# Optimization experiments

Measured on AMD Instinct MI355X. Metric: run time of the kernel, lower is better.

## Reference

```python
import jax, jax.numpy as jnp
import numpy as np

D_EMB = 256


def setup_inputs() -> dict:
    key = jax.random.key(0)
    ks = jax.random.split(key, 7)
    B, S, d = 4, 4096, D_EMB
    scale = 1.0 / np.sqrt(d)
    return {
        "x": jax.random.normal(ks[0], (B, S, d), jnp.float32),
        "Wqkv": jax.random.normal(ks[1], (d, 3 * d), jnp.float32) * scale,
        "bqkv": jax.random.normal(ks[2], (3 * d,), jnp.float32) * 0.02,
        "Wproj": jax.random.normal(ks[3], (d, d), jnp.float32) * scale,
        "bproj": jax.random.normal(ks[4], (d,), jnp.float32) * 0.02,
        "Wfc": jax.random.normal(ks[5], (d, 1), jnp.float32) * scale,
        "bfc": jax.random.normal(ks[6], (1,), jnp.float32) * 0.02,
    }


def reference(x, Wqkv, bqkv, Wproj, bproj, Wfc, bfc):
    # qkv projection: [B,S,3d] -> split into q,k,v [B,S,d]
    qkv = x @ Wqkv + bqkv
    q, k, v = jnp.split(qkv, 3, axis=2)
    # full attention scores [B,S,S]; note: original applies NO 1/sqrt(d)
    # scaling (dead branch in source), 'traditional' softmax over last dim
    attn_scores = jnp.einsum("bqd,bkd->bqk", q, k)
    attn_weights = jax.nn.softmax(attn_scores, axis=-1)
    y = jnp.einsum("bqk,bkd->bqd", attn_weights, v)
    y = y @ Wproj + bproj
    out = y @ Wfc + bfc  # [B,S,1]
    return out
```

## Files before the change

kernel.cpp:

```cpp
#include <hip/hip_runtime.h>
#include <hip/hip_bf16.h>

#define BQ 4
#define SQ 4096
#define DQ 256
#define N3 768
#define KBLK 64
#define NITER (SQ / KBLK)
#define KHALF (NITER / 2)
#define LOG2E 1.44269504f
#define THR2 11.5415603f

typedef __attribute__((ext_vector_type(8))) _Float16 f16x8;
typedef __attribute__((ext_vector_type(4))) _Float16 f16x4;
typedef __attribute__((ext_vector_type(4))) float f32x4;
typedef __attribute__((ext_vector_type(4))) unsigned int u32x4;

__device__ __forceinline__ short f2h(float f) {
  _Float16 h = (_Float16)f;
  union { _Float16 h; short s; } v; v.h = h;
  return v.s;
}

__device__ __forceinline__ void gload16(const void* g, void* lds) {
  __builtin_amdgcn_global_load_lds(
      (const __attribute__((address_space(1))) unsigned int*)g,
      (__attribute__((address_space(3))) unsigned int*)lds, 16, 0, 0);
}

__global__ __launch_bounds__(256) void prep_kernel(
    const float* __restrict__ Wqkv, const float* __restrict__ Wproj,
    const float* __restrict__ bproj, const float* __restrict__ Wfc,
    const float* __restrict__ bfc, short* __restrict__ W16T,
    float* __restrict__ Wc) {
  const int t = threadIdx.x;
  if (blockIdx.x == 48) {
    __shared__ float wf[256];
    wf[t] = Wfc[t];
    __syncthreads();
    float acc = 0.f;
    for (int j = 0; j < 256; ++j) acc += Wproj[(size_t)t * 256 + j] * wf[j];
    Wc[t] = acc;
    if (t == 0) {
      float c = bfc[0];
      for (int j = 0; j < 256; ++j) c += bproj[j] * wf[j];
      Wc[256] = c;
    }
    return;
  }
  __shared__ float tile[64][65];
  const int nb = (blockIdx.x % 12) * 64;
  const int kb = (blockIdx.x / 12) * 64;
  const int tr = t >> 6, tc = t & 63;
#pragma unroll
  for (int i = 0; i < 16; ++i)
    tile[tr + i * 4][tc] = Wqkv[(size_t)(kb + tr + i * 4) * N3 + nb + tc];
  __syncthreads();
#pragma unroll
  for (int i = 0; i < 16; ++i)
    W16T[(size_t)(nb + tr + i * 4) * 256 + kb + tc] = f2h(tile[tc][tr + i * 4]);
}

__global__ __launch_bounds__(1024, 4) void qkv_kernel(
    const float* __restrict__ x, const short* __restrict__ W16T,
    const float* __restrict__ bqkv, const float* __restrict__ Wc,
    short* __restrict__ Qb, short* __restrict__ Kb, short* __restrict__ u16) {
  __shared__ short xs[64][264];
  __shared__ short ws[2][64][256];
  __shared__ float u_red[4][4][16];
  const int t = threadIdx.x;
  const int l = t & 63, w = t >> 6;
  const int lr = l & 15, lg = l >> 4;
  const int mq = w >> 2, nq = w & 3;
  const int Mbase = blockIdx.x * 64;

#define STAGE_W(BUF, NT)                                                      \
  {                                                                           \
    _Pragma("unroll") for (int i = 0; i < 2; ++i) {                           \
      const int n = w * 4 + i * 2 + (l >> 5);                                 \
      const int gc = (l & 31) ^ (n & 7);                                      \
      gload16(W16T + (size_t)((NT)*64 + n) * 256 + gc * 8,                    \
              &ws[BUF][w * 4 + i * 2][0]);                                    \
    }                                                                         \
  }

  STAGE_W(0, 0);

  {
    const int m = t >> 4, kc = (t & 15) * 16;
    const float* src = x + (size_t)(Mbase + m) * DQ + kc;
    short tmp[16];
#pragma unroll
    for (int i = 0; i < 16; ++i) tmp[i] = f2h(src[i]);
    *(u32x4*)&xs[m][kc] = *(u32x4*)&tmp[0];
    *(u32x4*)&xs[m][kc + 8] = *(u32x4*)&tmp[8];
  }

  float bias_qk[8], bias_u[4], wc_u[4];
#pragma unroll
  for (int i = 0; i < 8; ++i) bias_qk[i] = bqkv[i * 64 + nq * 16 + lr];
#pragma unroll
  for (int i = 0; i < 4; ++i) {
    bias_u[i] = bqkv[512 + i * 64 + nq * 16 + lr];
    wc_u[i] = Wc[i * 64 + nq * 16 + lr];
  }

  __syncthreads();

  unsigned qksto[8][2];
  float upart[4] = {0.f, 0.f, 0.f, 0.f};

#pragma unroll
  for (int nt = 0; nt < 12; ++nt) {
    const int cur = nt & 1;
    if (nt + 1 < 12) {
      STAGE_W(cur ^ 1, nt + 1);
      asm volatile("s_waitcnt vmcnt(2)" ::: "memory");
    } else {
      asm volatile("s_waitcnt vmcnt(0)" ::: "memory");
    }
    __builtin_amdgcn_s_barrier();
    __builtin_amdgcn_sched_barrier(0);

    f32x4 acc = {};
    const char* wR = (const char*)&ws[cur][nq * 16 + lr][0];
#pragma unroll
    for (int kk = 0; kk < 8; ++kk) {
      f16x8 af = *(f16x8*)&xs[mq * 16 + lr][kk * 32 + lg * 8];
      f16x8 bfr = *(const f16x8*)(wR + (((4 * kk + lg) ^ (lr & 7)) << 4));
      acc = __builtin_amdgcn_mfma_f32_16x16x32_f16(af, bfr, acc, 0, 0, 0);
    }
    if (nt < 8) {
      const float sc = (nt < 4) ? 1.f : LOG2E;
      unsigned s0 = (unsigned short)f2h((acc[0] + bias_qk[nt]) * sc);
      unsigned s1 = (unsigned short)f2h((acc[1] + bias_qk[nt]) * sc);
      unsigned s2 = (unsigned short)f2h((acc[2] + bias_qk[nt]) * sc);
      unsigned s3 = (unsigned short)f2h((acc[3] + bias_qk[nt]) * sc);
      qksto[nt][0] = s0 | (s1 << 16);
      qksto[nt][1] = s2 | (s3 << 16);
    } else {
#pragma unroll
      for (int r = 0; r < 4; ++r) upart[r] += (acc[r] + bias_u[nt - 8]) * wc_u[nt - 8];
    }
    __builtin_amdgcn_s_barrier();
  }

#pragma unroll
  for (int nt = 0; nt < 8; ++nt) {
    const int col = nt * 64 + nq * 16 + lr;
#pragma unroll
    for (int r = 0; r < 4; ++r) {
      const int row = Mbase + mq * 16 + lg * 4 + r;
      const short sv = (short)((qksto[nt][r >> 1] >> ((r & 1) * 16)) & 0xFFFF);
      if (col < 256) Qb[(size_t)row * DQ + col] = sv;
      else           Kb[(size_t)row * DQ + (col - 256)] = sv;
    }
  }

#pragma unroll
  for (int mask = 1; mask <= 8; mask <<= 1)
#pragma unroll
    for (int r = 0; r < 4; ++r) upart[r] += __shfl_xor(upart[r], mask, 64);
  if (lr == 0) {
#pragma unroll
    for (int r = 0; r < 4; ++r) u_red[mq][nq][lg * 4 + r] = upart[r];
  }
  __syncthreads();
  if (t < 64)
    u16[Mbase + t] = f2h(u_red[t >> 4][0][t & 15] + u_red[t >> 4][1][t & 15] +
                         u_red[t >> 4][2][t & 15] + u_red[t >> 4][3][t & 15]);
#undef STAGE_W
}

__global__ __launch_bounds__(256, 2) void attn_kernel(
    const short* __restrict__ Qb, const short* __restrict__ Kb,
    const short* __restrict__ u16, float* __restrict__ Pm,
    float* __restrict__ Pd, float* __restrict__ Pn) {
  __shared__ short Ks[2][64][256];
  __shared__ __align__(16) short u_lds[2048];
  __shared__ float Mrg[4][64][3];

  const int t = threadIdx.x;
  const int l = t & 63, w = t >> 6;
  const int lr = l & 15, lg = l >> 4;
  const int bid = blockIdx.x;
  const int b = bid & 3;
  const int half = (bid >> 2) & 1;
  const int qbase = (bid >> 3) * 64;

  const short* kbase = Kb + ((size_t)b * SQ + (size_t)half * (SQ / 2)) * DQ;
  const short* ubase = u16 + (size_t)b * SQ + half * (SQ / 2);

#define STAGE(BUF, KB)                                                      \
  {                                                                         \
    _Pragma("unroll") for (int i = 0; i < 8; ++i) {                         \
      const int kr = w * 16 + i * 2 + (l >> 5);                             \
      const int gc = (l & 31) ^ (kr & 7);                                   \
      gload16(kbase + (size_t)((KB)*64 + kr) * DQ + gc * 8,                 \
              &Ks[BUF][w * 16 + i * 2][0]);                                 \
    }                                                                       \
  }

  {
    const short* qsrc = Qb + (size_t)(b * SQ + qbase) * DQ;
#pragma unroll
    for (int i = 0; i < 8; ++i) {
      const int qr = w * 16 + i * 2 + (l >> 5);
      const int gc = (l & 31) ^ (qr & 7);
      gload16(qsrc + (size_t)qr * DQ + gc * 8, &Ks[0][w * 16 + i * 2][0]);
    }
  }
  gload16(ubase + w * 512 + (l << 3), &u_lds[w * 512]);

  int koff[8];
#pragma unroll
  for (int kk = 0; kk < 8; ++kk) koff[kk] = ((4 * kk + lg) ^ (lr & 7)) << 4;

  asm volatile("s_waitcnt vmcnt(0)" ::: "memory");
  __syncthreads();

  f16x8 qf[4][8];
#pragma unroll
  for (int mm = 0; mm < 4; ++mm) {
    const char* qR = (const char*)&Ks[0][mm * 16 + lr][0];
#pragma unroll
    for (int kk = 0; kk < 8; ++kk)
      qf[mm][kk] = *(const f16x8*)(qR + koff[kk]);
  }
  __syncthreads();

  float m_run[4] = {-1e30f, -1e30f, -1e30f, -1e30f};
  f32x4 numden[4] = {};

  STAGE(0, 0);

  for (int kb = 0; kb < KHALF; ++kb) {
    const int cur = kb & 1;
    asm volatile("s_waitcnt vmcnt(0)" ::: "memory");
    __builtin_amdgcn_s_barrier();
    __builtin_amdgcn_sched_barrier(0);
    if (kb + 1 < KHALF) STAGE(cur ^ 1, kb + 1);

    const char* kR = (const char*)&Ks[cur][w * 16 + lr][0];
    f32x4 s[4] = {};
    __builtin_amdgcn_s_setprio(1);
#pragma unroll
    for (int kk = 0; kk < 8; ++kk) {
      f16x8 kf = *(const f16x8*)(kR + koff[kk]);
      s[0] = __builtin_amdgcn_mfma_f32_16x16x32_f16(kf, qf[0][kk], s[0], 0, 0, 0);
      s[1] = __builtin_amdgcn_mfma_f32_16x16x32_f16(kf, qf[1][kk], s[1], 0, 0, 0);
      s[2] = __builtin_amdgcn_mfma_f32_16x16x32_f16(kf, qf[2][kk], s[2], 0, 0, 0);
      s[3] = __builtin_amdgcn_mfma_f32_16x16x32_f16(kf, qf[3][kk], s[3], 0, 0, 0);
    }
    __builtin_amdgcn_s_setprio(0);

    float mx[4];
#pragma unroll
    for (int mm = 0; mm < 4; ++mm)
      mx[mm] = fmaxf(fmaxf(s[mm][0], s[mm][1]), fmaxf(s[mm][2], s[mm][3]));
    const bool over = (mx[0] > m_run[0] + THR2) || (mx[1] > m_run[1] + THR2) ||
                      (mx[2] > m_run[2] + THR2) || (mx[3] > m_run[3] + THR2);
    if (__any(over)) {
#pragma unroll
      for (int mm = 0; mm < 4; ++mm) {
        float mt = mx[mm];
        mt = fmaxf(mt, __shfl_xor(mt, 16, 64));
        mt = fmaxf(mt, __shfl_xor(mt, 32, 64));
        const float mn = fmaxf(m_run[mm], mt);
        const float sc = __builtin_amdgcn_exp2f(m_run[mm] - mn);
        m_run[mm] = mn;
#pragma unroll
        for (int r = 0; r < 4; ++r) numden[mm][r] *= sc;
      }
    }

    f16x4 uf;
    {
      const f16x4 uraw = *(const f16x4*)&u_lds[kb * 64 + w * 16 + lg * 4];
#pragma unroll
      for (int j = 0; j < 4; ++j)
        uf[j] = (lr == 0) ? uraw[j]
                          : ((lr == 1) ? (_Float16)1.0f : (_Float16)0.0f);
    }

#pragma unroll
    for (int mm = 0; mm < 4; ++mm) {
      const float p0 = __builtin_amdgcn_exp2f(s[mm][0] - m_run[mm]);
      const float p1 = __builtin_amdgcn_exp2f(s[mm][1] - m_run[mm]);
      const float p2 = __builtin_amdgcn_exp2f(s[mm][2] - m_run[mm]);
      const float p3 = __builtin_amdgcn_exp2f(s[mm][3] - m_run[mm]);
      const auto lo = __builtin_amdgcn_cvt_pkrtz(p0, p1);
      const auto hi = __builtin_amdgcn_cvt_pkrtz(p2, p3);
      f16x4 pf;
      pf[0] = (_Float16)lo[0]; pf[1] = (_Float16)lo[1];
      pf[2] = (_Float16)hi[0]; pf[3] = (_Float16)hi[1];
      numden[mm] = __builtin_amdgcn_mfma_f32_16x16x16f16(uf, pf, numden[mm], 0, 0, 0);
    }
  }

  if (lg == 0) {
#pragma unroll
    for (int mm = 0; mm < 4; ++mm) {
      Mrg[w][mm * 16 + lr][0] = m_run[mm];
      Mrg[w][mm * 16 + lr][1] = numden[mm][1];
      Mrg[w][mm * 16 + lr][2] = numden[mm][0];
    }
  }
  __syncthreads();

  if (t < 64) {
    float M = Mrg[0][t][0];
#pragma unroll
    for (int hh = 1; hh < 4; ++hh) M = fmaxf(M, Mrg[hh][t][0]);
    float dt = 0.f, nt = 0.f;
#pragma unroll
    for (int hh = 0; hh < 4; ++hh) {
      const float e = __builtin_amdgcn_exp2f(Mrg[hh][t][0] - M);
      dt += e * Mrg[hh][t][1];
      nt += e * Mrg[hh][t][2];
    }
    const size_t idx = (size_t)half * (BQ * SQ) + (size_t)b * SQ + qbase + t;
    Pm[idx] = M; Pd[idx] = dt; Pn[idx] = nt;
  }
#undef STAGE
}

__global__ void merge_kernel(const float* __restrict__ Pm,
                             const float* __restrict__ Pd,
                             const float* __restrict__ Pn,
                             const float* __restrict__ Wc,
                             float* __restrict__ out) {
  const int gid = blockIdx.x * 256 + threadIdx.x;
  const float m0 = Pm[gid], m1 = Pm[BQ * SQ + gid];
  const float M = fmaxf(m0, m1);
  const float e0 = __builtin_amdgcn_exp2f(m0 - M);
  const float e1 = __builtin_amdgcn_exp2f(m1 - M);
  const float den = e0 * Pd[gid] + e1 * Pd[BQ * SQ + gid];
  const float num = e0 * Pn[gid] + e1 * Pn[BQ * SQ + gid];
  out[gid] = num / den + Wc[256];
}

extern "C" void kernel_launch(void* const* d_in, const int* in_sizes, int n_in,
                              void* d_out, int out_size, void* d_ws, size_t ws_size,
                              hipStream_t stream) {
  const float* x     = (const float*)d_in[0];
  const float* Wqkv  = (const float*)d_in[1];
  const float* bqkv  = (const float*)d_in[2];
  const float* Wproj = (const float*)d_in[3];
  const float* bproj = (const float*)d_in[4];
  const float* Wfc   = (const float*)d_in[5];
  const float* bfc   = (const float*)d_in[6];
  float* out = (float*)d_out;

  const size_t SEG = (size_t)BQ * SQ * DQ * 2;
  char* wsb = (char*)d_ws;
  short* Qb   = (short*)(wsb);
  short* Kb   = (short*)(wsb + SEG);
  char* base  = wsb + 2 * SEG;
  float* Wc   = (float*)(base);
  short* u16  = (short*)(base + 4096);
  short* W16T = (short*)(base + 4096 + 65536);
  float* Pm   = (float*)(base + 4096 + 65536 + 393216);
  float* Pd   = Pm + 2 * BQ * SQ;
  float* Pn   = Pd + 2 * BQ * SQ;

  prep_kernel<<<49, 256, 0, stream>>>(Wqkv, Wproj, bproj, Wfc, bfc, W16T, Wc);
  qkv_kernel<<<256, 1024, 0, stream>>>(x, W16T, bqkv, Wc, Qb, Kb, u16);
  attn_kernel<<<512, 256, 0, stream>>>(Qb, Kb, u16, Pm, Pd, Pn);
  merge_kernel<<<BQ * SQ / 256, 256, 0, stream>>>(Pm, Pd, Pn, Wc, out);
}
```

Measured before the change: 92.65 us.

## Shrink QKV projection tiles to 32 rows with swizzled LDS and single barrier

The QKV projection kernel now processes 32 rows per block with 512 threads and launches 512 blocks instead of 256, so more blocks spread across CUs. The x tile in LDS gets an XOR swizzle matching the weight layout, with precomputed offsets, to avoid bank conflicts. The loop now uses one barrier per step and issues the next weight prefetch after it. LDS is packed into one aliased buffer that is reused for the reduction. In exchange, each block's weight staging is spread over fewer rows, so weight traffic per output row doubles, and the prefetch overlaps less with compute.

```diff
diff --git a/kernel.cpp b/kernel.cpp
--- a/kernel.cpp
+++ b/kernel.cpp
@@ -61,39 +61,39 @@
     W16T[(size_t)(nb + tr + i * 4) * 256 + kb + tc] = f2h(tile[tc][tr + i * 4]);
 }
 
-__global__ __launch_bounds__(1024, 4) void qkv_kernel(
+__global__ __launch_bounds__(512, 2) void qkv_kernel(
     const float* __restrict__ x, const short* __restrict__ W16T,
     const float* __restrict__ bqkv, const float* __restrict__ Wc,
     short* __restrict__ Qb, short* __restrict__ Kb, short* __restrict__ u16) {
-  __shared__ short xs[64][264];
-  __shared__ short ws[2][64][256];
-  __shared__ float u_red[4][4][16];
+  __shared__ short S[40960];
+#define XSP(m, k) (&S[(m)*256 + (k)])
+#define WSP(bf, n, k) (&S[8192 + (bf)*16384 + (n)*256 + (k)])
   const int t = threadIdx.x;
   const int l = t & 63, w = t >> 6;
   const int lr = l & 15, lg = l >> 4;
   const int mq = w >> 2, nq = w & 3;
-  const int Mbase = blockIdx.x * 64;
+  const int Mbase = blockIdx.x * 32;
 
 #define STAGE_W(BUF, NT)                                                      \
   {                                                                           \
-    _Pragma("unroll") for (int i = 0; i < 2; ++i) {                           \
-      const int n = w * 4 + i * 2 + (l >> 5);                                 \
+    _Pragma("unroll") for (int i = 0; i < 4; ++i) {                           \
+      const int n = w * 8 + i * 2 + (l >> 5);                                 \
       const int gc = (l & 31) ^ (n & 7);                                      \
       gload16(W16T + (size_t)((NT)*64 + n) * 256 + gc * 8,                    \
-              &ws[BUF][w * 4 + i * 2][0]);                                    \
+              WSP(BUF, w * 8 + i * 2, 0));                                    \
     }                                                                         \
   }
 
   STAGE_W(0, 0);
 
   {
-    const int m = t >> 4, kc = (t & 15) * 16;
-    const float* src = x + (size_t)(Mbase + m) * DQ + kc;
+    const int m = t >> 4, c = t & 15;
+    const float* src = x + (size_t)(Mbase + m) * DQ + c * 16;
     short tmp[16];
 #pragma unroll
     for (int i = 0; i < 16; ++i) tmp[i] = f2h(src[i]);
-    *(u32x4*)&xs[m][kc] = *(u32x4*)&tmp[0];
-    *(u32x4*)&xs[m][kc + 8] = *(u32x4*)&tmp[8];
+    *(u32x4*)XSP(m, ((2 * c) ^ (m & 7)) * 8) = *(u32x4*)&tmp[0];
+    *(u32x4*)XSP(m, ((2 * c + 1) ^ (m & 7)) * 8) = *(u32x4*)&tmp[8];
   }
 
   float bias_qk[8], bias_u[4], wc_u[4];
@@ -105,7 +105,9 @@
     wc_u[i] = Wc[i * 64 + nq * 16 + lr];
   }
 
-  __syncthreads();
+  int koff[8];
+#pragma unroll
+  for (int kk = 0; kk < 8; ++kk) koff[kk] = ((4 * kk + lg) ^ (lr & 7)) << 4;
 
   unsigned qksto[8][2];
   float upart[4] = {0.f, 0.f, 0.f, 0.f};
@@ -113,21 +115,18 @@
 #pragma unroll
   for (int nt = 0; nt < 12; ++nt) {
     const int cur = nt & 1;
-    if (nt + 1 < 12) {
-      STAGE_W(cur ^ 1, nt + 1);
-      asm volatile("s_waitcnt vmcnt(2)" ::: "memory");
-    } else {
-      asm volatile("s_waitcnt vmcnt(0)" ::: "memory");
-    }
+    asm volatile("s_waitcnt vmcnt(0) lgkmcnt(0)" ::: "memory");
     __builtin_amdgcn_s_barrier();
     __builtin_amdgcn_sched_barrier(0);
+    if (nt + 1 < 12) STAGE_W(cur ^ 1, nt + 1);
 
     f32x4 acc = {};
-    const char* wR = (const char*)&ws[cur][nq * 16 + lr][0];
+    const char* xR = (const char*)XSP(mq * 16 + lr, 0);
+    const char* wR = (const char*)WSP(cur, nq * 16 + lr, 0);
 #pragma unroll
     for (int kk = 0; kk < 8; ++kk) {
-      f16x8 af = *(f16x8*)&xs[mq * 16 + lr][kk * 32 + lg * 8];
-      f16x8 bfr = *(const f16x8*)(wR + (((4 * kk + lg) ^ (lr & 7)) << 4));
+      f16x8 af = *(const f16x8*)(xR + koff[kk]);
+      f16x8 bfr = *(const f16x8*)(wR + koff[kk]);
       acc = __builtin_amdgcn_mfma_f32_16x16x32_f16(af, bfr, acc, 0, 0, 0);
     }
     if (nt < 8) {
@@ -142,7 +141,6 @@
 #pragma unroll
       for (int r = 0; r < 4; ++r) upart[r] += (acc[r] + bias_u[nt - 8]) * wc_u[nt - 8];
     }
-    __builtin_amdgcn_s_barrier();
   }
 
 #pragma unroll
@@ -161,15 +159,24 @@
   for (int mask = 1; mask <= 8; mask <<= 1)
 #pragma unroll
     for (int r = 0; r < 4; ++r) upart[r] += __shfl_xor(upart[r], mask, 64);
+  __syncthreads();
+  float* u_red = (float*)&S[0];
   if (lr == 0) {
 #pragma unroll
-    for (int r = 0; r < 4; ++r) u_red[mq][nq][lg * 4 + r] = upart[r];
-  }
-  __syncthreads();
-  if (t < 64)
-    u16[Mbase + t] = f2h(u_red[t >> 4][0][t & 15] + u_red[t >> 4][1][t & 15] +
-                         u_red[t >> 4][2][t & 15] + u_red[t >> 4][3][t & 15]);
+    for (int r = 0; r < 4; ++r)
+      u_red[(mq * 4 + nq) * 16 + lg * 4 + r] = upart[r];
+  }
+  __syncthreads();
+  if (t < 32) {
+    const int g = t >> 4, row = t & 15;
+    u16[Mbase + t] = f2h(u_red[(g * 4 + 0) * 16 + row] +
+                         u_red[(g * 4 + 1) * 16 + row] +
+                         u_red[(g * 4 + 2) * 16 + row] +
+                         u_red[(g * 4 + 3) * 16 + row]);
+  }
 #undef STAGE_W
+#undef XSP
+#undef WSP
 }
 
 __global__ __launch_bounds__(256, 2) void attn_kernel(
@@ -365,7 +372,7 @@
   float* Pn   = Pd + 2 * BQ * SQ;
 
   prep_kernel<<<49, 256, 0, stream>>>(Wqkv, Wproj, bproj, Wfc, bfc, W16T, Wc);
-  qkv_kernel<<<256, 1024, 0, stream>>>(x, W16T, bqkv, Wc, Qb, Kb, u16);
+  qkv_kernel<<<512, 512, 0, stream>>>(x, W16T, bqkv, Wc, Qb, Kb, u16);
   attn_kernel<<<512, 256, 0, stream>>>(Qb, Kb, u16, Pm, Pd, Pn);
   merge_kernel<<<BQ * SQ / 256, 256, 0, stream>>>(Pm, Pd, Pn, Wc, out);
 }
```

Measured after the change: 92.09 us, median of 2. About the same (-0.6%).

## Retile QKV GEMM over 2D grid with pre-converted fp16 x and split u reduction

Applied to the files above, without the earlier changes.

The x-to-fp16 conversion moves into the prep kernel, which writes an x16 buffer. The QKV projection becomes a conventional 2D-tiled GEMM over 128x64 output tiles on a 128x12 grid, replacing one 64-row block that walked all 768 columns. Both operands are double-buffered through LDS via global_load_lds. The u-vector dot product is now reduced per column tile into partial sums, which a new small kernel combines. This raises parallelism and spreads the load better, at the cost of an extra launch, an extra x16 round trip through memory, and re-reading x tiles across 12 column blocks.

```diff
diff --git a/kernel.cpp b/kernel.cpp
--- a/kernel.cpp
+++ b/kernel.cpp
@@ -31,9 +31,17 @@
 __global__ __launch_bounds__(256) void prep_kernel(
     const float* __restrict__ Wqkv, const float* __restrict__ Wproj,
     const float* __restrict__ bproj, const float* __restrict__ Wfc,
-    const float* __restrict__ bfc, short* __restrict__ W16T,
-    float* __restrict__ Wc) {
+    const float* __restrict__ bfc, const float* __restrict__ x,
+    short* __restrict__ W16T, float* __restrict__ Wc,
+    short* __restrict__ x16) {
   const int t = threadIdx.x;
+  if (blockIdx.x >= 49) {
+    const size_t base = (size_t)(blockIdx.x - 49) * 16384;
+#pragma unroll 4
+    for (int i = 0; i < 64; ++i)
+      x16[base + i * 256 + t] = f2h(x[base + i * 256 + t]);
+    return;
+  }
   if (blockIdx.x == 48) {
     __shared__ float wf[256];
     wf[t] = Wfc[t];
@@ -61,115 +69,130 @@
     W16T[(size_t)(nb + tr + i * 4) * 256 + kb + tc] = f2h(tile[tc][tr + i * 4]);
 }
 
-__global__ __launch_bounds__(1024, 4) void qkv_kernel(
-    const float* __restrict__ x, const short* __restrict__ W16T,
+__global__ __launch_bounds__(512, 3) void qkv_kernel(
+    const short* __restrict__ x16, const short* __restrict__ W16T,
     const float* __restrict__ bqkv, const float* __restrict__ Wc,
-    short* __restrict__ Qb, short* __restrict__ Kb, short* __restrict__ u16) {
-  __shared__ short xs[64][264];
-  __shared__ short ws[2][64][256];
-  __shared__ float u_red[4][4][16];
+    short* __restrict__ Qb, short* __restrict__ Kb,
+    float* __restrict__ u_part) {
+  __shared__ short As[2][128][64];
+  __shared__ short Bs[2][64][64];
+  __shared__ float u_red[4][2][2][16];
   const int t = threadIdx.x;
   const int l = t & 63, w = t >> 6;
   const int lr = l & 15, lg = l >> 4;
-  const int mq = w >> 2, nq = w & 3;
-  const int Mbase = blockIdx.x * 64;
-
-#define STAGE_W(BUF, NT)                                                      \
-  {                                                                           \
-    _Pragma("unroll") for (int i = 0; i < 2; ++i) {                           \
-      const int n = w * 4 + i * 2 + (l >> 5);                                 \
-      const int gc = (l & 31) ^ (n & 7);                                      \
-      gload16(W16T + (size_t)((NT)*64 + n) * 256 + gc * 8,                    \
-              &ws[BUF][w * 4 + i * 2][0]);                                    \
-    }                                                                         \
-  }
-
-  STAGE_W(0, 0);
-
-  {
-    const int m = t >> 4, kc = (t & 15) * 16;
-    const float* src = x + (size_t)(Mbase + m) * DQ + kc;
-    short tmp[16];
-#pragma unroll
-    for (int i = 0; i < 16; ++i) tmp[i] = f2h(src[i]);
-    *(u32x4*)&xs[m][kc] = *(u32x4*)&tmp[0];
-    *(u32x4*)&xs[m][kc + 8] = *(u32x4*)&tmp[8];
-  }
-
-  float bias_qk[8], bias_u[4], wc_u[4];
-#pragma unroll
-  for (int i = 0; i < 8; ++i) bias_qk[i] = bqkv[i * 64 + nq * 16 + lr];
-#pragma unroll
-  for (int i = 0; i < 4; ++i) {
-    bias_u[i] = bqkv[512 + i * 64 + nq * 16 + lr];
-    wc_u[i] = Wc[i * 64 + nq * 16 + lr];
-  }
-
-  __syncthreads();
-
-  unsigned qksto[8][2];
-  float upart[4] = {0.f, 0.f, 0.f, 0.f};
-
-#pragma unroll
-  for (int nt = 0; nt < 12; ++nt) {
-    const int cur = nt & 1;
-    if (nt + 1 < 12) {
-      STAGE_W(cur ^ 1, nt + 1);
-      asm volatile("s_waitcnt vmcnt(2)" ::: "memory");
-    } else {
-      asm volatile("s_waitcnt vmcnt(0)" ::: "memory");
-    }
+  const int mq = w >> 1, nq = w & 1;
+  const int Mbase = blockIdx.x * 128;
+  const int bn = blockIdx.y;
+  const int Nbase = bn * 64;
+
+#define STAGE_AB(BUF, KS)                                                   \
+  {                                                                         \
+    _Pragma("unroll") for (int i = 0; i < 2; ++i) {                         \
+      const int ar = w * 16 + i * 8 + (l >> 3);                             \
+      const int gc = (l & 7) ^ (ar & 7);                                    \
+      gload16(x16 + (size_t)(Mbase + ar) * 256 + (KS)*64 + gc * 8,          \
+              &As[BUF][w * 16 + i * 8][0]);                                 \
+    }                                                                       \
+    {                                                                       \
+      const int br = w * 8 + (l >> 3);                                      \
+      const int gc = (l & 7) ^ (br & 7);                                    \
+      gload16(W16T + (size_t)(Nbase + br) * 256 + (KS)*64 + gc * 8,         \
+              &Bs[BUF][w * 8][0]);                                          \
+    }                                                                       \
+  }
+
+  STAGE_AB(0, 0);
+
+  float bias_v[2], wc_v[2] = {0.f, 0.f};
+#pragma unroll
+  for (int nf = 0; nf < 2; ++nf) {
+    const int col = Nbase + nq * 32 + nf * 16 + lr;
+    bias_v[nf] = bqkv[col];
+    if (bn >= 8) wc_v[nf] = Wc[col - 512];
+  }
+
+  int koff[2];
+#pragma unroll
+  for (int kk = 0; kk < 2; ++kk) koff[kk] = ((4 * kk + lg) ^ (lr & 7)) << 4;
+
+  f32x4 acc[2][2] = {};
+
+#pragma unroll
+  for (int ks = 0; ks < 4; ++ks) {
+    const int cur = ks & 1;
+    asm volatile("s_waitcnt vmcnt(0)" ::: "memory");
     __builtin_amdgcn_s_barrier();
     __builtin_amdgcn_sched_barrier(0);
-
-    f32x4 acc = {};
-    const char* wR = (const char*)&ws[cur][nq * 16 + lr][0];
-#pragma unroll
-    for (int kk = 0; kk < 8; ++kk) {
-      f16x8 af = *(f16x8*)&xs[mq * 16 + lr][kk * 32 + lg * 8];
-      f16x8 bfr = *(const f16x8*)(wR + (((4 * kk + lg) ^ (lr & 7)) << 4));
-      acc = __builtin_amdgcn_mfma_f32_16x16x32_f16(af, bfr, acc, 0, 0, 0);
-    }
-    if (nt < 8) {
-      const float sc = (nt < 4) ? 1.f : LOG2E;
-      unsigned s0 = (unsigned short)f2h((acc[0] + bias_qk[nt]) * sc);
-      unsigned s1 = (unsigned short)f2h((acc[1] + bias_qk[nt]) * sc);
-      unsigned s2 = (unsigned short)f2h((acc[2] + bias_qk[nt]) * sc);
-      unsigned s3 = (unsigned short)f2h((acc[3] + bias_qk[nt]) * sc);
-      qksto[nt][0] = s0 | (s1 << 16);
-      qksto[nt][1] = s2 | (s3 << 16);
-    } else {
-#pragma unroll
-      for (int r = 0; r < 4; ++r) upart[r] += (acc[r] + bias_u[nt - 8]) * wc_u[nt - 8];
-    }
-    __builtin_amdgcn_s_barrier();
-  }
-
-#pragma unroll
-  for (int nt = 0; nt < 8; ++nt) {
-    const int col = nt * 64 + nq * 16 + lr;
-#pragma unroll
-    for (int r = 0; r < 4; ++r) {
-      const int row = Mbase + mq * 16 + lg * 4 + r;
-      const short sv = (short)((qksto[nt][r >> 1] >> ((r & 1) * 16)) & 0xFFFF);
-      if (col < 256) Qb[(size_t)row * DQ + col] = sv;
-      else           Kb[(size_t)row * DQ + (col - 256)] = sv;
-    }
-  }
-
-#pragma unroll
-  for (int mask = 1; mask <= 8; mask <<= 1)
-#pragma unroll
-    for (int r = 0; r < 4; ++r) upart[r] += __shfl_xor(upart[r], mask, 64);
-  if (lr == 0) {
-#pragma unroll
-    for (int r = 0; r < 4; ++r) u_red[mq][nq][lg * 4 + r] = upart[r];
-  }
-  __syncthreads();
-  if (t < 64)
-    u16[Mbase + t] = f2h(u_red[t >> 4][0][t & 15] + u_red[t >> 4][1][t & 15] +
-                         u_red[t >> 4][2][t & 15] + u_red[t >> 4][3][t & 15]);
-#undef STAGE_W
+    if (ks < 3) STAGE_AB(cur ^ 1, ks + 1);
+
+    const char* aR0 = (const char*)&As[cur][mq * 32 + lr][0];
+    const char* aR1 = (const char*)&As[cur][mq * 32 + 16 + lr][0];
+    const char* bR0 = (const char*)&Bs[cur][nq * 32 + lr][0];
+    const char* bR1 = (const char*)&Bs[cur][nq * 32 + 16 + lr][0];
+#pragma unroll
+    for (int kk = 0; kk < 2; ++kk) {
+      f16x8 a0 = *(const f16x8*)(aR0 + koff[kk]);
+      f16x8 a1 = *(const f16x8*)(aR1 + koff[kk]);
+      f16x8 b0 = *(const f16x8*)(bR0 + koff[kk]);
+      f16x8 b1 = *(const f16x8*)(bR1 + koff[kk]);
+      acc[0][0] = __builtin_amdgcn_mfma_f32_16x16x32_f16(a0, b0, acc[0][0], 0, 0, 0);
+      acc[0][1] = __builtin_amdgcn_mfma_f32_16x16x32_f16(a0, b1, acc[0][1], 0, 0, 0);
+      acc[1][0] = __builtin_amdgcn_mfma_f32_16x16x32_f16(a1, b0, acc[1][0], 0, 0, 0);
+      acc[1][1] = __builtin_amdgcn_mfma_f32_16x16x32_f16(a1, b1, acc[1][1], 0, 0, 0);
+    }
+  }
+
+  if (bn < 8) {
+    const float sc = (bn < 4) ? 1.f : LOG2E;
+#pragma unroll
+    for (int mf = 0; mf < 2; ++mf)
+#pragma unroll
+      for (int nf = 0; nf < 2; ++nf) {
+        const int col = Nbase + nq * 32 + nf * 16 + lr;
+#pragma unroll
+        for (int r = 0; r < 4; ++r) {
+          const int row = Mbase + mq * 32 + mf * 16 + lg * 4 + r;
+          const short sv = f2h((acc[mf][nf][r] + bias_v[nf]) * sc);
+          if (bn < 4) Qb[(size_t)row * DQ + col] = sv;
+          else        Kb[(size_t)row * DQ + (col - 256)] = sv;
+        }
+      }
+  } else {
+    float up[2][4] = {};
+#pragma unroll
+    for (int nf = 0; nf < 2; ++nf)
+#pragma unroll
+      for (int mf = 0; mf < 2; ++mf)
+#pragma unroll
+        for (int r = 0; r < 4; ++r)
+          up[mf][r] += (acc[mf][nf][r] + bias_v[nf]) * wc_v[nf];
+#pragma unroll
+    for (int mask = 1; mask <= 8; mask <<= 1)
+#pragma unroll
+      for (int mf = 0; mf < 2; ++mf)
+#pragma unroll
+        for (int r = 0; r < 4; ++r) up[mf][r] += __shfl_xor(up[mf][r], mask, 64);
+    if (lr == 0) {
+#pragma unroll
+      for (int mf = 0; mf < 2; ++mf)
+#pragma unroll
+        for (int r = 0; r < 4; ++r)
+          u_red[mq][nq][mf][lg * 4 + r] = up[mf][r];
+    }
+    __syncthreads();
+    if (t < 128)
+      u_part[(size_t)(bn - 8) * (BQ * SQ) + Mbase + t] =
+          u_red[t >> 5][0][(t >> 4) & 1][t & 15] +
+          u_red[t >> 5][1][(t >> 4) & 1][t & 15];
+  }
+#undef STAGE_AB
+}
+
+__global__ void uvec_kernel(const float* __restrict__ up,
+                            short* __restrict__ u16) {
+  const int i = blockIdx.x * 256 + threadIdx.x;
+  u16[i] = f2h(up[i] + up[BQ * SQ + i] + up[2 * BQ * SQ + i] +
+               up[3 * BQ * SQ + i]);
 }
 
 __global__ __launch_bounds__(256, 2) void attn_kernel(
@@ -354,18 +377,23 @@
 
   const size_t SEG = (size_t)BQ * SQ * DQ * 2;
   char* wsb = (char*)d_ws;
-  short* Qb   = (short*)(wsb);
-  short* Kb   = (short*)(wsb + SEG);
-  char* base  = wsb + 2 * SEG;
-  float* Wc   = (float*)(base);
-  short* u16  = (short*)(base + 4096);
-  short* W16T = (short*)(base + 4096 + 65536);
-  float* Pm   = (float*)(base + 4096 + 65536 + 393216);
-  float* Pd   = Pm + 2 * BQ * SQ;
-  float* Pn   = Pd + 2 * BQ * SQ;
-
-  prep_kernel<<<49, 256, 0, stream>>>(Wqkv, Wproj, bproj, Wfc, bfc, W16T, Wc);
-  qkv_kernel<<<256, 1024, 0, stream>>>(x, W16T, bqkv, Wc, Qb, Kb, u16);
+  short* Qb     = (short*)(wsb);
+  short* Kb     = (short*)(wsb + SEG);
+  short* x16    = (short*)(wsb + 2 * SEG);
+  char* base    = wsb + 3 * SEG;
+  float* Wc     = (float*)(base);
+  short* u16    = (short*)(base + 2048);
+  short* W16T   = (short*)(base + 2048 + 32768);
+  float* u_part = (float*)(base + 2048 + 32768 + 393216);
+  float* Pm     = (float*)(base + 2048 + 32768 + 393216 + 262144);
+  float* Pd     = Pm + 2 * BQ * SQ;
+  float* Pn     = Pd + 2 * BQ * SQ;
+
+  prep_kernel<<<305, 256, 0, stream>>>(Wqkv, Wproj, bproj, Wfc, bfc, x,
+                                       W16T, Wc, x16);
+  qkv_kernel<<<dim3(128, 12), 512, 0, stream>>>(x16, W16T, bqkv, Wc, Qb, Kb,
+                                                u_part);
+  uvec_kernel<<<BQ * SQ / 256, 256, 0, stream>>>(u_part, u16);
   attn_kernel<<<512, 256, 0, stream>>>(Qb, Kb, u16, Pm, Pd, Pn);
   merge_kernel<<<BQ * SQ / 256, 256, 0, stream>>>(Pm, Pd, Pn, Wc, out);
 }
```

Measured after the change: 92.05 us. Within noise of the previous version (-0.6%).
